# Performance work log

Hardware: AMD Instinct MI355X
Metric: run time of the kernel (lower is better)

Reference implementation:

```python
import jax, jax.numpy as jnp
import numpy as np

INT8_MAX = 127.0

def _quant_ste(x, axis):
    """Dynamic symmetric int8 fake-quant along `axis` (per-channel scales).
    Returns dequantized values; math matches int8 dot * scales (AQT-style)."""
    amax = jnp.max(jnp.abs(x), axis=axis, keepdims=True)
    scale = jnp.maximum(amax, 1e-6) / INT8_MAX
    q = jnp.clip(jnp.round(x / scale), -INT8_MAX, INT8_MAX)
    return q * scale

def setup_inputs() -> dict:
    key = jax.random.key(0)
    k1, k2 = jax.random.split(key)
    inputs = jax.random.normal(k1, (4, 2048, 4096), dtype=jnp.float32)
    kernel = jax.random.normal(k2, (4096, 4096), dtype=jnp.float32) * 0.02
    return {"inputs": inputs, "kernel": kernel}

def reference(inputs, kernel):
    # eqn: '...y,yz->...z' with quantized dot_general:
    # per-row (last-axis) dynamic int8 quant of activations,
    # per-output-column int8 quant of kernel, int8 matmul, dequant by scales.
    xq = _quant_ste(inputs, axis=-1)   # [B, S, D]
    kq = _quant_ste(kernel, axis=0)    # [D, F]
    return jnp.einsum('bsd,df->bsf', xq, kq)  # [B, S, F]
```

## Files before the change

### kernel.cpp

```cpp
#include <hip/hip_runtime.h>


#define M_DIM 8192
#define K_DIM 4096
#define N_DIM 4096

typedef int v4i __attribute__((ext_vector_type(4)));
typedef __attribute__((address_space(3))) void lds_void_t;
typedef const __attribute__((address_space(1))) void g_void_t;

__global__ void amax_pass(const float* __restrict__ X,
                          float* __restrict__ sx, float* __restrict__ sxinv,
                          const float* __restrict__ W,
                          float* __restrict__ part) {
  const int t = threadIdx.x;

  if (blockIdx.x < 128) {
    const int f4 = (blockIdx.x & 3) * 256 + t;
    const int slab = blockIdx.x >> 2;
    const float4* p = (const float4*)W + (size_t)slab * 128 * 1024 + f4;
    float4 a0 = {0.f, 0.f, 0.f, 0.f}, a1 = {0.f, 0.f, 0.f, 0.f};
#pragma unroll 8
    for (int i = 0; i < 64; ++i) {
      float4 u = p[(size_t)(2 * i) * 1024];
      float4 v = p[(size_t)(2 * i + 1) * 1024];
      a0.x = fmaxf(a0.x, fabsf(u.x));
      a0.y = fmaxf(a0.y, fabsf(u.y));
      a0.z = fmaxf(a0.z, fabsf(u.z));
      a0.w = fmaxf(a0.w, fabsf(u.w));
      a1.x = fmaxf(a1.x, fabsf(v.x));
      a1.y = fmaxf(a1.y, fabsf(v.y));
      a1.z = fmaxf(a1.z, fabsf(v.z));
      a1.w = fmaxf(a1.w, fabsf(v.w));
    }
    float4 r;
    r.x = fmaxf(a0.x, a1.x);
    r.y = fmaxf(a0.y, a1.y);
    r.z = fmaxf(a0.z, a1.z);
    r.w = fmaxf(a0.w, a1.w);
    ((float4*)part)[(size_t)slab * 1024 + f4] = r;
    return;
  }

  const int row = (blockIdx.x - 128) * 8 + (t >> 5);
  const int j = t & 31;
  const float4* xr = (const float4*)X + (size_t)row * 1024;
  float am = 0.f;
#pragma unroll 8
  for (int i = 0; i < 32; ++i) {
    float4 v = xr[j + 32 * i];
    am = fmaxf(am, fmaxf(fmaxf(fabsf(v.x), fabsf(v.y)),
                         fmaxf(fabsf(v.z), fabsf(v.w))));
  }
#pragma unroll
  for (int off = 16; off > 0; off >>= 1)
    am = fmaxf(am, __shfl_down(am, off, 32));
  if (j == 0) {
    float scale = fmaxf(am, 1e-6f) / 127.0f;
    sx[row] = scale;
    sxinv[row] = 1.0f / scale;
  }
}

__global__ void act_quant(const float* __restrict__ X,
                          const float* __restrict__ sxinv,
                          signed char* __restrict__ At) {
  const int t = threadIdx.x;
  const int row = t >> 4;
  const int j = t & 15;
  const int r0 = blockIdx.x * 16;
  const float inv = sxinv[r0 + row];
  const float4* xr = (const float4*)X + (size_t)(r0 + row) * 1024;
  signed char* tile = At + (size_t)blockIdx.x * 65536 + row * 16;
#pragma unroll 4
  for (int u = 0; u < 16; ++u) {
    const int s = u * 16 + j;
    unsigned int d[4];
#pragma unroll
    for (int c = 0; c < 4; ++c) {
      float4 v = xr[s * 4 + c];
      int q0 = (int)fminf(fmaxf(rintf(v.x * inv), -127.f), 127.f);
      int q1 = (int)fminf(fmaxf(rintf(v.y * inv), -127.f), 127.f);
      int q2 = (int)fminf(fmaxf(rintf(v.z * inv), -127.f), 127.f);
      int q3 = (int)fminf(fmaxf(rintf(v.w * inv), -127.f), 127.f);
      d[c] = (q0 & 255) | ((q1 & 255) << 8) | ((q2 & 255) << 16) | (q3 << 24);
    }
    v4i w = {(int)d[0], (int)d[1], (int)d[2], (int)d[3]};
    *(v4i*)(tile + s * 256) = w;
  }
}

__global__ void wk_quant(const float* __restrict__ W,
                         const float* __restrict__ part,
                         signed char* __restrict__ Bt,
                         float* __restrict__ sk) {
  const int bx = blockIdx.x;
  const int f0 = (bx & 63) * 64;
  const int d0 = (bx >> 6) * 64;
  const int t = threadIdx.x;
  const int fl4 = t & 15;
  const int dl0 = t >> 4;
  __shared__ __align__(16) signed char tile[64 * 80];
  __shared__ float sl_inv[64];

  float4 wv[4];
#pragma unroll
  for (int c = 0; c < 4; ++c) {
    const int dl = c * 16 + dl0;
    wv[c] = ((const float4*)W)[(size_t)(d0 + dl) * 1024 + (f0 >> 2) + fl4];
  }
  if (t < 64) {
    const int f = f0 + t;
    float m = 0.f;
#pragma unroll
    for (int s = 0; s < 32; ++s) m = fmaxf(m, part[(size_t)s * 4096 + f]);
    const float scale = fmaxf(m, 1e-6f) / 127.0f;
    if (bx < 64) sk[f] = scale;
    sl_inv[t] = 1.0f / scale;
  }
  __syncthreads();
  const float4 inv4 = *(const float4*)&sl_inv[fl4 * 4];
#pragma unroll
  for (int c = 0; c < 4; ++c) {
    const int dl = c * 16 + dl0;
    tile[(fl4 * 4 + 0) * 80 + dl] =
        (signed char)(int)fminf(fmaxf(rintf(wv[c].x * inv4.x), -127.f), 127.f);
    tile[(fl4 * 4 + 1) * 80 + dl] =
        (signed char)(int)fminf(fmaxf(rintf(wv[c].y * inv4.y), -127.f), 127.f);
    tile[(fl4 * 4 + 2) * 80 + dl] =
        (signed char)(int)fminf(fmaxf(rintf(wv[c].z * inv4.z), -127.f), 127.f);
    tile[(fl4 * 4 + 3) * 80 + dl] =
        (signed char)(int)fminf(fmaxf(rintf(wv[c].w * inv4.w), -127.f), 127.f);
  }
  __syncthreads();
  const int frow = t >> 2;
  const int ksl = t & 3;
  v4i w = *(const v4i*)&tile[frow * 80 + ksl * 16];
  const int f = f0 + frow;
  signed char* dst = Bt + (size_t)(f >> 4) * 65536 + ((d0 >> 4) + ksl) * 256 +
                     (f & 15) * 16;
  *(v4i*)dst = w;
}

__global__ __launch_bounds__(256, 2) void gemm_i8(
    const signed char* __restrict__ At, const signed char* __restrict__ Bt,
    const float* __restrict__ sx, const float* __restrict__ sk,
    float* __restrict__ C) {
  const int n0 = blockIdx.x * 128;
  const int m0 = blockIdx.y * 128;
  const int t = threadIdx.x;
  const int lane = t & 63;
  const int wave = t >> 6;
  const int wm = (wave >> 1) * 64;
  const int wn = (wave & 1) * 64;
  const int lrow = lane & 15;
  const int lq = lane >> 4;

  __shared__ __align__(16) signed char lds[32768];
  signed char* lA = lds;
  signed char* lB = lds + 16384;

  v4i acc[4][4];
#pragma unroll
  for (int i = 0; i < 4; ++i)
#pragma unroll
    for (int j = 0; j < 4; ++j) acc[i][j] = (v4i){0, 0, 0, 0};

  const signed char* Abase = At + (size_t)(m0 >> 4) * 65536;
  const signed char* Bbase = Bt + (size_t)(n0 >> 4) * 65536;

  const int la = ((wave >> 1) * 4) * 2048 + lane * 16;
  const int lb = ((wave & 1) * 4) * 2048 + lane * 16;

  for (int kb = 0; kb < K_DIM; kb += 128) {
    const int kofs = kb * 16;
#pragma unroll
    for (int j = 0; j < 4; ++j) {
      const int c = j * 256 + t;
      const int mt_i = c >> 7;
      const int inner = c & 127;
      __builtin_amdgcn_global_load_lds(
          (g_void_t*)(Abase + (size_t)mt_i * 65536 + kofs + inner * 16),
          (lds_void_t*)(lA + c * 16), 16, 0, 0);
      __builtin_amdgcn_global_load_lds(
          (g_void_t*)(Bbase + (size_t)mt_i * 65536 + kofs + inner * 16),
          (lds_void_t*)(lB + c * 16), 16, 0, 0);
    }
    __syncthreads();
#pragma unroll
    for (int s = 0; s < 2; ++s) {
      v4i af[4], bf[4];
#pragma unroll
      for (int i = 0; i < 4; ++i) af[i] = *(const v4i*)(lA + la + i * 2048 + s * 1024);
#pragma unroll
      for (int i = 0; i < 4; ++i) bf[i] = *(const v4i*)(lB + lb + i * 2048 + s * 1024);
#pragma unroll
      for (int mi = 0; mi < 4; ++mi)
#pragma unroll
        for (int ni = 0; ni < 4; ++ni)
          acc[mi][ni] =
              __builtin_amdgcn_mfma_i32_16x16x64_i8(af[mi], bf[ni], acc[mi][ni], 0, 0, 0);
    }
    __syncthreads();
  }

#pragma unroll
  for (int mi = 0; mi < 4; ++mi) {
#pragma unroll
    for (int ni = 0; ni < 4; ++ni) {
      const int gn = n0 + wn + ni * 16 + lrow;
      const float skv = sk[gn];
#pragma unroll
      for (int r = 0; r < 4; ++r) {
        const int gm = m0 + wm + mi * 16 + lq * 4 + r;
        C[(size_t)gm * N_DIM + gn] = (float)acc[mi][ni][r] * sx[gm] * skv;
      }
    }
  }
}

extern "C" void kernel_launch(void* const* d_in, const int* in_sizes, int n_in,
                              void* d_out, int out_size, void* d_ws, size_t ws_size,
                              hipStream_t stream) {
  const float* X = (const float*)d_in[0];
  const float* W = (const float*)d_in[1];
  float* out = (float*)d_out;
  char* ws = (char*)d_ws;

  signed char* At = (signed char*)ws;
  signed char* Bt = (signed char*)(ws + 33554432);
  float* sx = (float*)(ws + 50331648);
  float* sxinv = (float*)(ws + 50364416);
  float* sk = (float*)(ws + 50397184);
  float* part = (float*)(ws + 50413568);

  amax_pass<<<1152, 256, 0, stream>>>(X, sx, sxinv, W, part);
  act_quant<<<512, 256, 0, stream>>>(X, sxinv, At);
  wk_quant<<<4096, 256, 0, stream>>>(W, part, Bt, sk);
  gemm_i8<<<dim3(N_DIM / 128, M_DIM / 128), 256, 0, stream>>>(At, Bt, sx, sk, out);
}
```

Measured before the change: 443.6 us.

## Use 256x256 tiles with double-buffered LDS pipeline and repacked int8 panels

```diff
diff --git a/kernel.cpp b/kernel.cpp
--- a/kernel.cpp
+++ b/kernel.cpp
@@ -4,6 +4,7 @@
 #define M_DIM 8192
 #define K_DIM 4096
 #define N_DIM 4096
+#define NT (K_DIM / 128)
 
 typedef int v4i __attribute__((ext_vector_type(4)));
 typedef __attribute__((address_space(3))) void lds_void_t;
@@ -69,9 +70,14 @@
   const int row = t >> 4;
   const int j = t & 15;
   const int r0 = blockIdx.x * 16;
+  const int mt = blockIdx.x & 15;
+  const int panel = blockIdx.x >> 4;
+  const int q = mt >> 2;
+  const int pq = ((q & 1) << 1) | (q >> 1);
+  const int p = (mt & 3) | (pq << 2);
   const float inv = sxinv[r0 + row];
   const float4* xr = (const float4*)X + (size_t)(r0 + row) * 1024;
-  signed char* tile = At + (size_t)blockIdx.x * 65536 + row * 16;
+  signed char* tile = At + (size_t)panel * 1048576 + (size_t)p * 65536 + row * 16;
 #pragma unroll 4
   for (int u = 0; u < 16; ++u) {
     const int s = u * 16 + j;
@@ -86,7 +92,7 @@
       d[c] = (q0 & 255) | ((q1 & 255) << 8) | ((q2 & 255) << 16) | (q3 << 24);
     }
     v4i w = {(int)d[0], (int)d[1], (int)d[2], (int)d[3]};
-    *(v4i*)(tile + s * 256) = w;
+    *(v4i*)(tile + (s >> 3) * 2048 + (s & 7) * 256) = w;
   }
 }
 
@@ -137,82 +143,128 @@
   const int ksl = t & 3;
   v4i w = *(const v4i*)&tile[frow * 80 + ksl * 16];
   const int f = f0 + frow;
-  signed char* dst = Bt + (size_t)(f >> 4) * 65536 + ((d0 >> 4) + ksl) * 256 +
-                     (f & 15) * 16;
+  const int lt = (f >> 4) & 15;
+  const int p = ((lt >> 1) & 1) * 8 + (lt >> 2) * 2 + (lt & 1);
+  const int s = (d0 >> 4) + ksl;
+  signed char* dst = Bt + (size_t)(f >> 8) * 1048576 + (size_t)p * 65536 +
+                     (s >> 3) * 2048 + (s & 7) * 256 + (f & 15) * 16;
   *(v4i*)dst = w;
 }
 
-__global__ __launch_bounds__(256, 2) void gemm_i8(
+#define SA(J, KT, STG)                                                        \
+  __builtin_amdgcn_global_load_lds(                                           \
+      (g_void_t*)(Ap + soff[J] + (size_t)(KT)*2048),                          \
+      (lds_void_t*)((STG) + ((J)*512 + t) * 16), 16, 0, 0)
+#define SB(J, KT, STG)                                                        \
+  __builtin_amdgcn_global_load_lds(                                           \
+      (g_void_t*)(Bp + soff[J] + (size_t)(KT)*2048),                          \
+      (lds_void_t*)((STG) + 32768 + ((J)*512 + t) * 16), 16, 0, 0)
+
+#define QPHASE(MQ, NQ, STAGE_STMT, WAIT_STMT)                                 \
+  do {                                                                        \
+    STAGE_STMT;                                                               \
+    v4i af[4][2], bf[2][2];                                                   \
+    _Pragma("unroll") for (int i = 0; i < 4; ++i) {                           \
+      const signed char* pa = lA + ((MQ)*8 + wam + i) * 2048 + lane * 16;     \
+      af[i][0] = *(const v4i*)pa;                                             \
+      af[i][1] = *(const v4i*)(pa + 1024);                                    \
+    }                                                                         \
+    _Pragma("unroll") for (int ni = 0; ni < 2; ++ni) {                        \
+      const signed char* pb = lB + ((NQ)*8 + wbn + ni) * 2048 + lane * 16;    \
+      bf[ni][0] = *(const v4i*)pb;                                            \
+      bf[ni][1] = *(const v4i*)(pb + 1024);                                   \
+    }                                                                         \
+    WAIT_STMT;                                                                \
+    asm volatile("s_barrier" ::: "memory");                                   \
+    __builtin_amdgcn_s_setprio(1);                                            \
+    _Pragma("unroll") for (int s2 = 0; s2 < 2; ++s2)                          \
+        _Pragma("unroll") for (int i = 0; i < 4; ++i)                         \
+            _Pragma("unroll") for (int ni = 0; ni < 2; ++ni)                  \
+                acc[(MQ)*4 + i][(NQ)*2 + ni] =                                \
+        __builtin_amdgcn_mfma_i32_16x16x64_i8(                                \
+            af[i][s2], bf[ni][s2], acc[(MQ)*4 + i][(NQ)*2 + ni], 0, 0, 0);    \
+    __builtin_amdgcn_s_setprio(0);                                            \
+    asm volatile("s_waitcnt lgkmcnt(0)" ::: "memory");                        \
+    asm volatile("s_barrier" ::: "memory");                                   \
+  } while (0)
+
+#define WAIT4 asm volatile("s_waitcnt vmcnt(4)" ::: "memory")
+#define WAIT2 asm volatile("s_waitcnt vmcnt(2)" ::: "memory")
+#define WAIT0 asm volatile("s_waitcnt vmcnt(0)" ::: "memory")
+
+__global__ __launch_bounds__(512, 2) void gemm_i8(
     const signed char* __restrict__ At, const signed char* __restrict__ Bt,
     const float* __restrict__ sx, const float* __restrict__ sk,
     float* __restrict__ C) {
-  const int n0 = blockIdx.x * 128;
-  const int m0 = blockIdx.y * 128;
+  const int n0 = blockIdx.x * 256;
+  const int m0 = blockIdx.y * 256;
   const int t = threadIdx.x;
   const int lane = t & 63;
   const int wave = t >> 6;
-  const int wm = (wave >> 1) * 64;
-  const int wn = (wave & 1) * 64;
+  const int wm = (wave >> 2) * 128;
+  const int wn = (wave & 3) * 64;
+  const int wam = (wave >> 2) * 4;
+  const int wbn = (wave & 3) * 2;
   const int lrow = lane & 15;
   const int lq = lane >> 4;
 
-  __shared__ __align__(16) signed char lds[32768];
-  signed char* lA = lds;
-  signed char* lB = lds + 16384;
-
-  v4i acc[4][4];
-#pragma unroll
-  for (int i = 0; i < 4; ++i)
+  __shared__ __align__(16) signed char lds[131072];
+
+  v4i acc[8][4];
+#pragma unroll
+  for (int i = 0; i < 8; ++i)
 #pragma unroll
     for (int j = 0; j < 4; ++j) acc[i][j] = (v4i){0, 0, 0, 0};
 
-  const signed char* Abase = At + (size_t)(m0 >> 4) * 65536;
-  const signed char* Bbase = Bt + (size_t)(n0 >> 4) * 65536;
-
-  const int la = ((wave >> 1) * 4) * 2048 + lane * 16;
-  const int lb = ((wave & 1) * 4) * 2048 + lane * 16;
-
-  for (int kb = 0; kb < K_DIM; kb += 128) {
-    const int kofs = kb * 16;
-#pragma unroll
-    for (int j = 0; j < 4; ++j) {
-      const int c = j * 256 + t;
-      const int mt_i = c >> 7;
-      const int inner = c & 127;
-      __builtin_amdgcn_global_load_lds(
-          (g_void_t*)(Abase + (size_t)mt_i * 65536 + kofs + inner * 16),
-          (lds_void_t*)(lA + c * 16), 16, 0, 0);
-      __builtin_amdgcn_global_load_lds(
-          (g_void_t*)(Bbase + (size_t)mt_i * 65536 + kofs + inner * 16),
-          (lds_void_t*)(lB + c * 16), 16, 0, 0);
-    }
-    __syncthreads();
-#pragma unroll
-    for (int s = 0; s < 2; ++s) {
-      v4i af[4], bf[4];
-#pragma unroll
-      for (int i = 0; i < 4; ++i) af[i] = *(const v4i*)(lA + la + i * 2048 + s * 1024);
-#pragma unroll
-      for (int i = 0; i < 4; ++i) bf[i] = *(const v4i*)(lB + lb + i * 2048 + s * 1024);
-#pragma unroll
-      for (int mi = 0; mi < 4; ++mi)
-#pragma unroll
-        for (int ni = 0; ni < 4; ++ni)
-          acc[mi][ni] =
-              __builtin_amdgcn_mfma_i32_16x16x64_i8(af[mi], bf[ni], acc[mi][ni], 0, 0, 0);
-    }
-    __syncthreads();
-  }
-
-#pragma unroll
-  for (int mi = 0; mi < 4; ++mi) {
+  const signed char* Ap = At + (size_t)(m0 >> 8) * 1048576;
+  const signed char* Bp = Bt + (size_t)(n0 >> 8) * 1048576;
+
+  int soff[4];
+#pragma unroll
+  for (int j = 0; j < 4; ++j)
+    soff[j] = (j * 4 + (t >> 7)) * 65536 + (t & 127) * 16;
+
+  {
+    signed char* stg = lds;
+    SA(0, 0, stg); SA(1, 0, stg);
+    SB(0, 0, stg); SB(1, 0, stg);
+    SA(2, 0, stg); SA(3, 0, stg);
+    SB(2, 0, stg); SB(3, 0, stg);
+  }
+  WAIT4;
+  asm volatile("s_barrier" ::: "memory");
+
+#pragma unroll 1
+  for (int kt = 0; kt < NT - 1; ++kt) {
+    const signed char* lA = lds + (kt & 1) * 65536;
+    const signed char* lB = lA + 32768;
+    signed char* stg = lds + (((kt & 1) ^ 1) * 65536);
+    const int nx = kt + 1;
+    QPHASE(0, 0, { SA(0, nx, stg); SA(1, nx, stg); }, WAIT4);
+    QPHASE(1, 0, { SB(0, nx, stg); SB(1, nx, stg); }, WAIT4);
+    QPHASE(0, 1, { SA(2, nx, stg); SA(3, nx, stg); }, );
+    QPHASE(1, 1, { SB(2, nx, stg); SB(3, nx, stg); }, WAIT4);
+  }
+
+  {
+    const signed char* lA = lds + ((NT - 1) & 1) * 65536;
+    const signed char* lB = lA + 32768;
+    QPHASE(0, 0, , WAIT2);
+    QPHASE(1, 0, , WAIT0);
+    QPHASE(0, 1, , );
+    QPHASE(1, 1, , );
+  }
+
+#pragma unroll
+  for (int mi = 0; mi < 8; ++mi) {
+    const int gmb = m0 + wm + (mi >> 2) * 64 + (mi & 3) * 16 + lq * 4;
 #pragma unroll
     for (int ni = 0; ni < 4; ++ni) {
-      const int gn = n0 + wn + ni * 16 + lrow;
+      const int gn = n0 + wn + (ni >> 1) * 32 + (ni & 1) * 16 + lrow;
       const float skv = sk[gn];
 #pragma unroll
       for (int r = 0; r < 4; ++r) {
-        const int gm = m0 + wm + mi * 16 + lq * 4 + r;
+        const int gm = gmb + r;
         C[(size_t)gm * N_DIM + gn] = (float)acc[mi][ni][r] * sx[gm] * skv;
       }
     }
@@ -237,5 +289,5 @@
   amax_pass<<<1152, 256, 0, stream>>>(X, sx, sxinv, W, part);
   act_quant<<<512, 256, 0, stream>>>(X, sxinv, At);
   wk_quant<<<4096, 256, 0, stream>>>(W, part, Bt, sk);
-  gemm_i8<<<dim3(N_DIM / 128, M_DIM / 128), 256, 0, stream>>>(At, Bt, sx, sk, out);
-}
+  gemm_i8<<<dim3(N_DIM / 256, M_DIM / 256), 512, 0, stream>>>(At, Bt, sx, sk, out);
+}
```

After: 440.4 us. No clear change (-0.7%).
